# Kernel tuning notes

Measured on AMD Instinct MI355X. Metric: run time of the kernel, lower is better.

The kernel has to match this reference:

```python
import jax, jax.numpy as jnp
import numpy as np

B = 16
T_LEN, T_DIM = 149, 768
H = W = 56
S_DIM = 512
EPS = 1e-5


def setup_inputs() -> dict:
    key = jax.random.key(0)
    ks = jax.random.split(key, 12)
    N = H * W  # 3136
    return {
        "x": jax.random.normal(ks[0], (B, T_LEN, T_DIM), dtype=jnp.float32),
        "y": jax.random.normal(ks[1], (B, S_DIM, H, W), dtype=jnp.float32),
        # Conv1d(time_len -> h*w, k=1)
        "W_conv1": jax.random.normal(ks[2], (N, T_LEN), dtype=jnp.float32) * (1.0 / np.sqrt(T_LEN)),
        "b_conv1": jnp.zeros((N,), dtype=jnp.float32),
        # LayerNorms
        "ln1_g": jnp.ones((T_DIM,), dtype=jnp.float32),
        "ln1_b": jnp.zeros((T_DIM,), dtype=jnp.float32),
        "ln2_g": jnp.ones((S_DIM,), dtype=jnp.float32),
        "ln2_b": jnp.zeros((S_DIM,), dtype=jnp.float32),
        # positional encodings (1, C, H, W)
        "pe_wave": jax.random.normal(ks[3], (1, T_DIM, H, W), dtype=jnp.float32) * 0.02,
        "pe_spec": jax.random.normal(ks[4], (1, S_DIM, H, W), dtype=jnp.float32) * 0.02,
        # CrossAttention2D 1x1 convs
        "Wq": jax.random.normal(ks[5], (S_DIM, T_DIM), dtype=jnp.float32) * (1.0 / np.sqrt(T_DIM)),
        "bq": jnp.zeros((S_DIM,), dtype=jnp.float32),
        "Wk": jax.random.normal(ks[6], (S_DIM, S_DIM), dtype=jnp.float32) * (1.0 / np.sqrt(S_DIM)),
        "bk": jnp.zeros((S_DIM,), dtype=jnp.float32),
    }


def _layernorm(t, g, b):
    # t: (..., C), normalized over last axis
    m = jnp.mean(t, axis=-1, keepdims=True)
    v = jnp.mean(jnp.square(t - m), axis=-1, keepdims=True)
    return (t - m) * jax.lax.rsqrt(v + EPS) * g + b


def reference(x, y, W_conv1, b_conv1, ln1_g, ln1_b, ln2_g, ln2_b,
              pe_wave, pe_spec, Wq, bq, Wk, bk):
    # conv1d k=1 over channel dim time_len: (B,149,768) -> (B,3136,768)
    xe = jnp.einsum('bld,ol->bod', x, W_conv1) + b_conv1[None, :, None]
    # rearrange 'b (h w) c -> b h w c' (channel-last for LN/attention)
    nx = xe.reshape(x.shape[0], H, W, T_DIM)
    nx = _layernorm(nx, ln1_g, ln1_b) + pe_wave.transpose(0, 2, 3, 1)  # (B,H,W,768)

    ny = y.transpose(0, 2, 3, 1)  # (B,H,W,512)
    ny = _layernorm(ny, ln2_g, ln2_b) + pe_spec.transpose(0, 2, 3, 1)

    # 1x1 convs -> q, k; value is norm_y itself
    q = jnp.einsum('bhwc,oc->bhwo', nx, Wq) + bq  # (B,H,W,512)
    k = jnp.einsum('bhwc,oc->bhwo', ny, Wk) + bk  # (B,H,W,512)
    v = ny

    # row-local attention: each (b,h) row of W=56 tokens attends within itself
    scores = jnp.einsum('bhqc,bhkc->bhqk', q, k) / jnp.sqrt(jnp.float32(S_DIM))
    attn = jax.nn.softmax(scores, axis=-1)  # (B,H,W,W)
    out = jnp.einsum('bhqk,bhkc->bhqc', attn, v)  # (B,H,W,512)

    # permute back to (B,C,H,W), residual add
    return out.transpose(0, 3, 1, 2) + y
```

## Files before the change

### kernel.cpp

```cpp
#include <hip/hip_runtime.h>
#include <hip/hip_bf16.h>
#include <math.h>

typedef short bf16x8 __attribute__((ext_vector_type(8)));
typedef float f32x4 __attribute__((ext_vector_type(4)));

#define LN_EPS 1e-5f

static __device__ __forceinline__ float b2f(unsigned short u){
  unsigned int x = ((unsigned int)u) << 16; float f; __builtin_memcpy(&f,&x,4); return f;
}
static __device__ __forceinline__ unsigned short f2b(float f){
  unsigned int x; __builtin_memcpy(&x,&f,4);
  x += 0x7fffu + ((x>>16)&1u);
  return (unsigned short)(x>>16);
}

static __device__ __forceinline__ void gload_lds16(const void* g, void* l){
  __builtin_amdgcn_global_load_lds(
      (const __attribute__((address_space(1))) unsigned int*)g,
      (__attribute__((address_space(3))) unsigned int*)l, 16, 0, 0);
}

#define MFMA16(a,b,c) __builtin_amdgcn_mfma_f32_16x16x32_bf16(a,b,c,0,0,0)

__global__ void pack_rowpad(const float* __restrict__ src, unsigned short* __restrict__ dst,
                            int rows, int srcK, int dstK, int rowsPad){
  int idx = blockIdx.x*256 + threadIdx.x;
  if (idx >= rowsPad*dstK) return;
  int r = idx / dstK, kk = idx - r*dstK;
  float v = (r < rows && kk < srcK) ? src[(size_t)r*srcK + kk] : 0.f;
  dst[idx] = f2b(v);
}

__global__ __launch_bounds__(256) void pack_xt(const float* __restrict__ x, unsigned short* __restrict__ xt){
  __shared__ float tile[32][33];
  int b = blockIdx.z;
  int l0 = blockIdx.y*32, d0 = blockIdx.x*32;
  int tl = threadIdx.x & 31, tw = threadIdx.x >> 5;
  for (int r=0;r<32;r+=8){
    int l = l0 + tw + r;
    tile[tw+r][tl] = (l<149) ? x[((size_t)b*149 + l)*768 + d0 + tl] : 0.f;
  }
  __syncthreads();
  for (int r=0;r<32;r+=8){
    int d = d0 + tw + r;
    int l = l0 + tl;
    if (l < 160) xt[((size_t)b*768 + d)*160 + l] = f2b(tile[tl][tw+r]);
  }
}

__global__ __launch_bounds__(256) void transpose_pe(const float* __restrict__ src, float* __restrict__ dst, int C){
  __shared__ float tile[32][33];
  int c0 = blockIdx.y*32, o0 = blockIdx.x*32;
  int tl = threadIdx.x & 31, tw = threadIdx.x >> 5;
  for (int r=0;r<32;r+=8)
    tile[tw+r][tl] = src[(size_t)(c0+tw+r)*3136 + o0 + tl];
  __syncthreads();
  for (int r=0;r<32;r+=8)
    dst[(size_t)(o0+tw+r)*C + c0 + tl] = tile[tl][tw+r];
}

__global__ __launch_bounds__(256)
void conv160(const unsigned short* __restrict__ A, const unsigned short* __restrict__ Bt,
             unsigned short* __restrict__ C, int M, int N,
             long long bStride, long long cStride){
  __shared__ __align__(16) unsigned short lds[40960];
  const int K = 160;
  int tid = threadIdx.x;
  int lane = tid & 63, wave = tid >> 6;
  int wm = (wave >> 1)*64, wn = (wave & 1)*64;
  int lr = lane & 15, lo = lane >> 4;
  int m0 = blockIdx.x*128, n0 = blockIdx.y*128;
  const unsigned short* Bb = Bt + (size_t)blockIdx.z*bStride;
  unsigned short* Cb = C + (size_t)blockIdx.z*cStride;

  #pragma unroll
  for (int i=0;i<20;i++){
    int cbase = i*256 + wave*64;
    int tensor = (cbase >= 2560) ? 1 : 0;
    int ccb = cbase - tensor*2560;
    int cc = ccb + lane;
    int r = cc / 20, pc = cc - r*20;
    int sw = (r ^ (r >> 2)) & 3;
    int ps = pc ^ sw;
    const unsigned short* srcT = tensor ? (Bb + (size_t)n0*K) : (A + (size_t)m0*K);
    gload_lds16(srcT + (size_t)r*K + ps*8, lds + tensor*20480 + ccb*8);
  }
  asm volatile("s_waitcnt vmcnt(0)" ::: "memory");
  __builtin_amdgcn_s_barrier();

  f32x4 acc[4][4];
  #pragma unroll
  for (int i=0;i<4;i++)
    #pragma unroll
    for (int j=0;j<4;j++) acc[i][j]=(f32x4){0.f,0.f,0.f,0.f};
  #pragma unroll
  for (int kk=0; kk<5; ++kk){
    bf16x8 af[4], bfr[4];
    #pragma unroll
    for (int mi=0;mi<4;mi++){
      int row = wm + mi*16 + lr;
      int p = kk*4 + (lo ^ ((row ^ (row>>2)) & 3));
      af[mi] = *reinterpret_cast<const bf16x8*>(&lds[row*160 + p*8]);
    }
    #pragma unroll
    for (int nj=0;nj<4;nj++){
      int row = wn + nj*16 + lr;
      int p = kk*4 + (lo ^ ((row ^ (row>>2)) & 3));
      bfr[nj] = *reinterpret_cast<const bf16x8*>(&lds[20480 + row*160 + p*8]);
    }
    #pragma unroll
    for (int mi=0;mi<4;mi++)
      #pragma unroll
      for (int nj=0;nj<4;nj++)
        acc[mi][nj] = MFMA16(af[mi], bfr[nj], acc[mi][nj]);
  }
  int er = lo*4;
  #pragma unroll
  for (int mi=0;mi<4;mi++)
    #pragma unroll
    for (int nj=0;nj<4;nj++){
      int col = n0 + wn + nj*16 + lr;
      #pragma unroll
      for (int e=0;e<4;e++){
        int row = m0 + wm + mi*16 + er + e;
        if (row < M) Cb[(size_t)row*N + col] = f2b(acc[mi][nj][e]);
      }
    }
}

__global__ __launch_bounds__(512)
void gemm256_bk32(const unsigned short* __restrict__ A, const unsigned short* __restrict__ Bt,
                  unsigned short* __restrict__ C, const float* __restrict__ bias,
                  int M, int N, int K){
  __shared__ __align__(16) unsigned short lds[32768];
  int tid = threadIdx.x;
  int lane = tid & 63, wave = tid >> 6;
  int wr = wave >> 2, wc = wave & 3;
  int lr = lane & 15, lo = lane >> 4;
  int cpx = gridDim.x >> 3;
  int id = blockIdx.x;
  int sid = (id & 7)*cpx + (id >> 3);
  int nby = N >> 8;
  int bx = sid / nby, by = sid - bx*nby;
  int m0 = bx << 8, n0 = by << 8;
  int NT = K >> 5;

  f32x4 acc[8][4];
  #pragma unroll
  for (int i=0;i<8;i++)
    #pragma unroll
    for (int j=0;j<4;j++) acc[i][j]=(f32x4){0.f,0.f,0.f,0.f};

  auto STAGE = [&](int t){
    if (t >= NT) return;
    int buf = t & 1;
    int k0 = t << 5;
    #pragma unroll
    for (int i=0;i<4;i++){
      int cbase = i*512 + wave*64;
      int tensor = cbase >> 10;
      int ccb = cbase & 1023;
      int cc = ccb + lane;
      int r = cc >> 2, pc = cc & 3;
      int ps = pc ^ ((r ^ (r >> 2)) & 3);
      const unsigned short* srcT = tensor ? (Bt + (size_t)n0*K) : (A + (size_t)m0*K);
      gload_lds16(srcT + (size_t)r*K + k0 + ps*8, lds + buf*16384 + tensor*8192 + ccb*8);
    }
  };
  auto rdA = [&](int buf, int mi)->bf16x8{
    int row = wr*128 + mi*16 + lr;
    int p = lo ^ ((row ^ (row >> 2)) & 3);
    return *reinterpret_cast<const bf16x8*>(&lds[buf*16384 + row*32 + p*8]);
  };
  auto rdB = [&](int buf, int nj)->bf16x8{
    int row = wc*64 + nj*16 + lr;
    int p = lo ^ ((row ^ (row >> 2)) & 3);
    return *reinterpret_cast<const bf16x8*>(&lds[buf*16384 + 8192 + row*32 + p*8]);
  };

  STAGE(0);
  asm volatile("s_waitcnt vmcnt(0)" ::: "memory");
  __builtin_amdgcn_s_barrier();

  for (int t=0; t<NT; ++t){
    int buf = t & 1;
    STAGE(t+1);
    bf16x8 bfr[4], af[4];
    #pragma unroll
    for (int nj=0;nj<4;nj++) bfr[nj] = rdB(buf,nj);
    #pragma unroll
    for (int i=0;i<4;i++) af[i] = rdA(buf,i);
    asm volatile("s_waitcnt lgkmcnt(0)" ::: "memory");
    __builtin_amdgcn_sched_barrier(0);
    __builtin_amdgcn_s_setprio(1);
    #pragma unroll
    for (int i=0;i<4;i++)
      #pragma unroll
      for (int nj=0;nj<4;nj++)
        acc[i][nj] = MFMA16(af[i], bfr[nj], acc[i][nj]);
    __builtin_amdgcn_s_setprio(0);
    #pragma unroll
    for (int i=0;i<4;i++) af[i] = rdA(buf,4+i);
    asm volatile("s_waitcnt lgkmcnt(0)" ::: "memory");
    __builtin_amdgcn_sched_barrier(0);
    __builtin_amdgcn_s_setprio(1);
    #pragma unroll
    for (int i=0;i<4;i++)
      #pragma unroll
      for (int nj=0;nj<4;nj++)
        acc[4+i][nj] = MFMA16(af[i], bfr[nj], acc[4+i][nj]);
    __builtin_amdgcn_s_setprio(0);
    asm volatile("s_waitcnt vmcnt(0)" ::: "memory");
    __builtin_amdgcn_s_barrier();
  }

  int er = lo*4;
  #pragma unroll
  for (int nj=0;nj<4;nj++){
    int col = n0 + wc*64 + nj*16 + lr;
    float bv = bias ? bias[col] : 0.f;
    #pragma unroll
    for (int mi=0;mi<8;mi++){
      int row = m0 + wr*128 + mi*16 + er;
      #pragma unroll
      for (int e=0;e<4;e++)
        C[(size_t)(row+e)*N + col] = f2b(acc[mi][nj][e] + bv);
    }
  }
}

__global__ __launch_bounds__(256) void ln1_kernel(unsigned short* __restrict__ xe,
    const float* __restrict__ g, const float* __restrict__ be, const float* __restrict__ pet){
  int b = blockIdx.y;
  int o0 = blockIdx.x*8;
  int t = threadIdx.x;
  int lane = t & 63, wv = t >> 6;
  __shared__ float ws1[8][4], ws2[8][4];
  __shared__ float mArr[8], rArr[8];
  float vals[8][3];
  #pragma unroll
  for (int oi=0;oi<8;oi++){
    size_t base = ((size_t)b*3136 + o0 + oi)*768;
    #pragma unroll
    for (int j=0;j<3;j++) vals[oi][j] = b2f(xe[base + t + 256*j]);
  }
  #pragma unroll
  for (int oi=0;oi<8;oi++){
    float s1=0.f, s2=0.f;
    #pragma unroll
    for (int j=0;j<3;j++){ float v=vals[oi][j]; s1+=v; s2+=v*v; }
    #pragma unroll
    for (int d=32; d>0; d>>=1){ s1 += __shfl_xor(s1,d); s2 += __shfl_xor(s2,d); }
    if (lane==0){ ws1[oi][wv]=s1; ws2[oi][wv]=s2; }
  }
  __syncthreads();
  if (t < 8){
    float a = ws1[t][0]+ws1[t][1]+ws1[t][2]+ws1[t][3];
    float c = ws2[t][0]+ws2[t][1]+ws2[t][2]+ws2[t][3];
    float m = a*(1.f/768.f);
    float var = c*(1.f/768.f) - m*m;
    mArr[t] = m; rArr[t] = rsqrtf(var + LN_EPS);
  }
  __syncthreads();
  #pragma unroll
  for (int oi=0;oi<8;oi++){
    size_t base = ((size_t)b*3136 + o0 + oi)*768;
    size_t pb = (size_t)(o0+oi)*768;
    float m=mArr[oi], r=rArr[oi];
    #pragma unroll
    for (int j=0;j<3;j++){
      int d = t + 256*j;
      xe[base+d] = f2b((vals[oi][j]-m)*r*g[d] + be[d] + pet[pb+d]);
    }
  }
}

__global__ __launch_bounds__(256) void ln2_kernel(const float* __restrict__ y,
    unsigned short* __restrict__ ny, unsigned short* __restrict__ nyT,
    const float* __restrict__ g, const float* __restrict__ bb, const float* __restrict__ pe){
  int b = blockIdx.y;
  int o0 = blockIdx.x*32;
  int t = threadIdx.x;
  int oi = t & 31, cg = t >> 5;
  __shared__ float red1[8][33], red2[8][33];
  __shared__ float mArr[32], rArr[32];
  __shared__ unsigned short tile[32][520];
  size_t ybase = (size_t)b*512*3136 + o0;
  float vals[64];
  float s1=0.f, s2=0.f;
  #pragma unroll
  for (int ci=0; ci<64; ci++){
    int c = cg*64 + ci;
    float v = y[ybase + (size_t)c*3136 + oi];
    vals[ci] = v;
    s1 += v; s2 += v*v;
  }
  red1[cg][oi]=s1; red2[cg][oi]=s2;
  __syncthreads();
  if (t < 32){
    float a=0.f, c2=0.f;
    #pragma unroll
    for (int kk=0;kk<8;kk++){ a+=red1[kk][t]; c2+=red2[kk][t]; }
    float m=a*(1.f/512.f);
    float var=c2*(1.f/512.f)-m*m;
    mArr[t]=m; rArr[t]=rsqrtf(var+LN_EPS);
  }
  __syncthreads();
  float m = mArr[oi], r = rArr[oi];
  #pragma unroll
  for (int ci=0; ci<64; ci++){
    int c = cg*64 + ci;
    float v = (vals[ci]-m)*r*g[c] + bb[c] + pe[(size_t)c*3136 + o0 + oi];
    tile[oi][c] = f2b(v);
  }
  __syncthreads();
  size_t nybase = ((size_t)b*3136 + o0)*512;
  for (int p = t; p < 32*64; p += 256){
    int oo = p >> 6, cp = (p & 63)*8;
    *reinterpret_cast<uint4*>(ny + nybase + (size_t)oo*512 + cp) =
        *reinterpret_cast<const uint4*>(&tile[oo][cp]);
  }
  for (int c2 = t; c2 < 512; c2 += 256){
    unsigned short row[32];
    #pragma unroll
    for (int o=0;o<32;o++) row[o] = tile[o][c2];
    size_t a = ((size_t)b*512 + c2)*3136 + o0;
    #pragma unroll
    for (int u=0;u<4;u++)
      *reinterpret_cast<uint4*>(nyT + a + u*8) = *reinterpret_cast<const uint4*>(&row[u*8]);
  }
}

__global__ __launch_bounds__(512) void attn_kernel(const unsigned short* __restrict__ q,
    const unsigned short* __restrict__ k, const unsigned short* __restrict__ vT,
    const float* __restrict__ y, float* __restrict__ outp){
  int id = blockIdx.x;
  int sid = (id & 7)*112 + (id >> 3);
  int b = sid / 56, h = sid - b*56;
  int tid = threadIdx.x;
  int lane = tid & 63, w = tid >> 6;
  int wc = w & 3, wk = w >> 2;
  size_t base = (size_t)b*3136 + (size_t)h*56;
  __shared__ __align__(16) float SfP[2][56][60];
  __shared__ __align__(16) unsigned short Sb[64*64];

  f32x4 acc[4];
  #pragma unroll
  for (int mi=0;mi<4;mi++) acc[mi]=(f32x4){0.f,0.f,0.f,0.f};
  int lr = lane & 15, lo = lane >> 4;
  int lk = lo*8;
  int kr = wc*16 + lr; if (kr > 55) kr = 55;
  const unsigned short* krow = k + (base + kr)*512 + wk*256;
  const unsigned short* qrow = q + base*512 + wk*256;
  #pragma unroll
  for (int k0=0;k0<256;k0+=32){
    bf16x8 kf = *reinterpret_cast<const bf16x8*>(krow + k0 + lk);
    #pragma unroll
    for (int mi=0;mi<4;mi++){
      int qr = mi*16 + lr; if (qr > 55) qr = 55;
      bf16x8 qf = *reinterpret_cast<const bf16x8*>(qrow + (size_t)qr*512 + k0 + lk);
      acc[mi] = __builtin_amdgcn_mfma_f32_16x16x32_bf16(qf, kf, acc[mi], 0,0,0);
    }
  }

  const unsigned short* vb = vT + (size_t)b*512*3136 + (size_t)h*56;
  bf16x8 vfr[2][2][2];
  #pragma unroll
  for (int hp=0; hp<2; ++hp)
    #pragma unroll
    for (int kt=0;kt<2;++kt)
      #pragma unroll
      for (int mi=0;mi<2;++mi){
        int d = w*64 + hp*32 + mi*16 + lr;
        vfr[hp][kt][mi] = *reinterpret_cast<const bf16x8*>(vb + (size_t)d*3136 + kt*32 + lk);
      }

  int col = wc*16 + lr;
  int er = lo*4;
  if (col < 56){
    #pragma unroll
    for (int mi=0;mi<4;mi++)
      #pragma unroll
      for (int e=0;e<4;e++){
        int row = mi*16 + er + e;
        if (row < 56) SfP[wk][row][col] = acc[mi][e];
      }
  }
  __syncthreads();

  const float scale = 0.04419417382415922f;
  for (int r=0;r<7;r++){
    int i = w*7 + r;
    float xv = (lane<56) ? (SfP[0][i][lane] + SfP[1][i][lane])*scale : -1e30f;
    float mx = xv;
    #pragma unroll
    for (int d=32; d>0; d>>=1) mx = fmaxf(mx, __shfl_xor(mx,d));
    float ev = (lane<56) ? __expf(xv-mx) : 0.f;
    float sm = ev;
    #pragma unroll
    for (int d=32; d>0; d>>=1) sm += __shfl_xor(sm,d);
    unsigned short pv = (lane<56) ? f2b(ev/sm) : (unsigned short)0;
    int bo = i*128 + ((lane*2) ^ ((i&7)<<4));
    *reinterpret_cast<unsigned short*>(reinterpret_cast<char*>(Sb) + bo) = pv;
  }
  __syncthreads();

  bf16x8 pf[2][4];
  #pragma unroll
  for (int kt=0;kt<2;++kt)
    #pragma unroll
    for (int nj=0;nj<4;++nj){
      int row = nj*16 + lr;
      int bo = row*128 + (((kt*64) + lo*16) ^ ((row&7)<<4));
      pf[kt][nj] = *reinterpret_cast<const bf16x8*>(reinterpret_cast<const char*>(Sb) + bo);
    }

  #pragma unroll
  for (int hp=0; hp<2; ++hp){
    f32x4 a2[2][4];
    #pragma unroll
    for (int mi=0;mi<2;mi++)
      #pragma unroll
      for (int nj=0;nj<4;nj++) a2[mi][nj]=(f32x4){0.f,0.f,0.f,0.f};
    #pragma unroll
    for (int kt=0;kt<2;++kt)
      #pragma unroll
      for (int mi=0;mi<2;++mi)
        #pragma unroll
        for (int nj=0;nj<4;++nj)
          a2[mi][nj] = __builtin_amdgcn_mfma_f32_16x16x32_bf16(vfr[hp][kt][mi], pf[kt][nj], a2[mi][nj], 0,0,0);
    #pragma unroll
    for (int mi=0;mi<2;++mi)
      #pragma unroll
      for (int e=0;e<4;++e){
        size_t rowb = ((size_t)b*512 + w*64 + hp*32 + mi*16 + er + e)*3136 + (size_t)h*56;
        #pragma unroll
        for (int nj=0;nj<4;++nj){
          int r = nj*16 + lr;
          if (r < 56) outp[rowb + r] = a2[mi][nj][e] + y[rowb + r];
        }
      }
  }
}

extern "C" void kernel_launch(void* const* d_in, const int* in_sizes, int n_in,
                              void* d_out, int out_size, void* d_ws, size_t ws_size,
                              hipStream_t stream){
  const float* x   = (const float*)d_in[0];
  const float* y   = (const float*)d_in[1];
  const float* Wc  = (const float*)d_in[2];
  const float* g1  = (const float*)d_in[4];
  const float* be1 = (const float*)d_in[5];
  const float* g2  = (const float*)d_in[6];
  const float* be2 = (const float*)d_in[7];
  const float* peW = (const float*)d_in[8];
  const float* peS = (const float*)d_in[9];
  const float* Wq  = (const float*)d_in[10];
  const float* bq  = (const float*)d_in[11];
  const float* Wk  = (const float*)d_in[12];
  const float* bk  = (const float*)d_in[13];
  float* outp = (float*)d_out;

  char* p = (char*)d_ws;
  auto alloc = [&](size_t bytes)->char*{ char* r = p; p += (bytes + 255) & ~(size_t)255; return r; };
  unsigned short* WcB = (unsigned short*)alloc((size_t)3200*160*2);
  unsigned short* xt  = (unsigned short*)alloc((size_t)16*768*160*2);
  unsigned short* WqB = (unsigned short*)alloc((size_t)512*768*2);
  unsigned short* WkB = (unsigned short*)alloc((size_t)512*512*2);
  float* peWt = (float*)alloc((size_t)3136*768*4);
  unsigned short* xe  = (unsigned short*)alloc((size_t)16*3136*768*2);
  unsigned short* ny  = (unsigned short*)alloc((size_t)16*3136*512*2);
  unsigned short* nyT = (unsigned short*)alloc((size_t)16*512*3136*2 + 256);
  unsigned short* qb  = (unsigned short*)alloc((size_t)16*3136*512*2);
  unsigned short* kb  = (unsigned short*)alloc((size_t)16*3136*512*2);

  pack_rowpad<<<dim3((3200*160+255)/256), 256, 0, stream>>>(Wc, WcB, 3136, 149, 160, 3200);
  pack_rowpad<<<dim3((512*768+255)/256), 256, 0, stream>>>(Wq, WqB, 512, 768, 768, 512);
  pack_rowpad<<<dim3((512*512+255)/256), 256, 0, stream>>>(Wk, WkB, 512, 512, 512, 512);
  pack_xt<<<dim3(24,5,16), 256, 0, stream>>>(x, xt);
  transpose_pe<<<dim3(98,24), 256, 0, stream>>>(peW, peWt, 768);

  conv160<<<dim3(25,6,16), 256, 0, stream>>>(WcB, xt, xe, 3136, 768,
                                             768LL*160LL, 3136LL*768LL);
  ln1_kernel<<<dim3(392,16), 256, 0, stream>>>(xe, g1, be1, peWt);
  ln2_kernel<<<dim3(98,16), 256, 0, stream>>>(y, ny, nyT, g2, be2, peS);
  gemm256_bk32<<<dim3(392), 512, 0, stream>>>(xe, WqB, qb, bq, 50176, 512, 768);
  gemm256_bk32<<<dim3(392), 512, 0, stream>>>(ny, WkB, kb, bk, 50176, 512, 512);
  attn_kernel<<<dim3(896), 512, 0, stream>>>(qb, kb, nyT, y, outp);
}
```

Measured before the change: 389.9 us.

## Split attention blocks across value-channel halves with 256-thread blocks

The attention kernel now launches twice as many 256-thread blocks. Each block handles one (b,h) row and one half of the 512 output channels, instead of one 512-thread block per row that split the score reduction across two wave groups. Each block recomputes the full QK^T scores over all 512 channels itself, which removes the cross-wave partial-sum reduction in shared memory. The cost is twice the Q/K loads and score MFMAs overall. It also zero-pads unused P rows explicitly and batches the Q fragment loads before the MFMAs.

```diff
diff --git a/kernel.cpp b/kernel.cpp
--- a/kernel.cpp
+++ b/kernel.cpp
@@ -333,17 +333,17 @@
   }
 }
 
-__global__ __launch_bounds__(512) void attn_kernel(const unsigned short* __restrict__ q,
+__global__ __launch_bounds__(256) void attn_kernel(const unsigned short* __restrict__ q,
     const unsigned short* __restrict__ k, const unsigned short* __restrict__ vT,
     const float* __restrict__ y, float* __restrict__ outp){
   int id = blockIdx.x;
-  int sid = (id & 7)*112 + (id >> 3);
-  int b = sid / 56, h = sid - b*56;
+  int sid = (id & 7)*224 + (id >> 3);
+  int pair = sid >> 1, dhalf = sid & 1;
+  int b = pair / 56, h = pair - b*56;
   int tid = threadIdx.x;
   int lane = tid & 63, w = tid >> 6;
-  int wc = w & 3, wk = w >> 2;
   size_t base = (size_t)b*3136 + (size_t)h*56;
-  __shared__ __align__(16) float SfP[2][56][60];
+  __shared__ __align__(16) float Sf[56][60];
   __shared__ __align__(16) unsigned short Sb[64*64];
 
   f32x4 acc[4];
@@ -351,18 +351,21 @@
   for (int mi=0;mi<4;mi++) acc[mi]=(f32x4){0.f,0.f,0.f,0.f};
   int lr = lane & 15, lo = lane >> 4;
   int lk = lo*8;
-  int kr = wc*16 + lr; if (kr > 55) kr = 55;
-  const unsigned short* krow = k + (base + kr)*512 + wk*256;
-  const unsigned short* qrow = q + base*512 + wk*256;
-  #pragma unroll
-  for (int k0=0;k0<256;k0+=32){
+  int kr = w*16 + lr; if (kr > 55) kr = 55;
+  const unsigned short* krow = k + (base + kr)*512;
+  const unsigned short* qrow = q + base*512;
+  #pragma unroll 4
+  for (int k0=0;k0<512;k0+=32){
     bf16x8 kf = *reinterpret_cast<const bf16x8*>(krow + k0 + lk);
+    bf16x8 qf[4];
     #pragma unroll
     for (int mi=0;mi<4;mi++){
       int qr = mi*16 + lr; if (qr > 55) qr = 55;
-      bf16x8 qf = *reinterpret_cast<const bf16x8*>(qrow + (size_t)qr*512 + k0 + lk);
-      acc[mi] = __builtin_amdgcn_mfma_f32_16x16x32_bf16(qf, kf, acc[mi], 0,0,0);
-    }
+      qf[mi] = *reinterpret_cast<const bf16x8*>(qrow + (size_t)qr*512 + k0 + lk);
+    }
+    #pragma unroll
+    for (int mi=0;mi<4;mi++)
+      acc[mi] = __builtin_amdgcn_mfma_f32_16x16x32_bf16(qf[mi], kf, acc[mi], 0,0,0);
   }
 
   const unsigned short* vb = vT + (size_t)b*512*3136 + (size_t)h*56;
@@ -373,11 +376,12 @@
     for (int kt=0;kt<2;++kt)
       #pragma unroll
       for (int mi=0;mi<2;++mi){
-        int d = w*64 + hp*32 + mi*16 + lr;
+        int d = dhalf*256 + w*64 + hp*32 + mi*16 + lr;
         vfr[hp][kt][mi] = *reinterpret_cast<const bf16x8*>(vb + (size_t)d*3136 + kt*32 + lk);
       }
 
-  int col = wc*16 + lr;
+  const float scale = 0.04419417382415922f;
+  int col = w*16 + lr;
   int er = lo*4;
   if (col < 56){
     #pragma unroll
@@ -385,15 +389,14 @@
       #pragma unroll
       for (int e=0;e<4;e++){
         int row = mi*16 + er + e;
-        if (row < 56) SfP[wk][row][col] = acc[mi][e];
+        if (row < 56) Sf[row][col] = acc[mi][e]*scale;
       }
   }
   __syncthreads();
 
-  const float scale = 0.04419417382415922f;
-  for (int r=0;r<7;r++){
-    int i = w*7 + r;
-    float xv = (lane<56) ? (SfP[0][i][lane] + SfP[1][i][lane])*scale : -1e30f;
+  for (int r=0;r<14;r++){
+    int i = w*14 + r;
+    float xv = (lane<56) ? Sf[i][lane] : -1e30f;
     float mx = xv;
     #pragma unroll
     for (int d=32; d>0; d>>=1) mx = fmaxf(mx, __shfl_xor(mx,d));
@@ -405,6 +408,12 @@
     int bo = i*128 + ((lane*2) ^ ((i&7)<<4));
     *reinterpret_cast<unsigned short*>(reinterpret_cast<char*>(Sb) + bo) = pv;
   }
+  #pragma unroll
+  for (int z=0; z<2; ++z){
+    int i = 56 + w*2 + z;
+    int bo = i*128 + ((lane*2) ^ ((i&7)<<4));
+    *reinterpret_cast<unsigned short*>(reinterpret_cast<char*>(Sb) + bo) = 0;
+  }
   __syncthreads();
 
   bf16x8 pf[2][4];
@@ -435,7 +444,7 @@
     for (int mi=0;mi<2;++mi)
       #pragma unroll
       for (int e=0;e<4;++e){
-        size_t rowb = ((size_t)b*512 + w*64 + hp*32 + mi*16 + er + e)*3136 + (size_t)h*56;
+        size_t rowb = ((size_t)b*512 + dhalf*256 + w*64 + hp*32 + mi*16 + er + e)*3136 + (size_t)h*56;
         #pragma unroll
         for (int nj=0;nj<4;++nj){
           int r = nj*16 + lr;
@@ -488,5 +497,5 @@
   ln2_kernel<<<dim3(98,16), 256, 0, stream>>>(y, ny, nyT, g2, be2, peS);
   gemm256_bk32<<<dim3(392), 512, 0, stream>>>(xe, WqB, qb, bq, 50176, 512, 768);
   gemm256_bk32<<<dim3(392), 512, 0, stream>>>(ny, WkB, kb, bk, 50176, 512, 512);
-  attn_kernel<<<dim3(896), 512, 0, stream>>>(qb, kb, nyT, y, outp);
-}
+  attn_kernel<<<dim3(1792), 256, 0, stream>>>(qb, kb, nyT, y, outp);
+}
```

Result: slower. 423.3 us (+8.6%).
